# Performance work log

Measured on AMD Instinct MI355X. Metric: run time of the kernel, lower is better.

The kernel has to match this reference:

```python
import jax, jax.numpy as jnp
import numpy as np
from jax import lax

B, T, N, C, AD, HW, KS, KT = 32, 8, 196, 768, 192, 14, 3, 3
EPS = 1e-5

def _groupnorm1(x, gamma, beta, axes):
    # GroupNorm(1, C): normalize over channel+spatial dims per sample
    mu = jnp.mean(x, axis=axes, keepdims=True)
    var = jnp.mean((x - mu) ** 2, axis=axes, keepdims=True)
    xn = (x - mu) * lax.rsqrt(var + EPS)
    shape = [1] * x.ndim
    shape[1] = -1
    return xn * gamma.reshape(shape) + beta.reshape(shape)

def setup_inputs() -> dict:
    key = jax.random.key(0)
    ks = jax.random.split(key, 16)
    s = 0.02
    return {
        'x': jax.random.normal(ks[0], (B, T, N + 1, C), jnp.float32),
        'w_down': jax.random.normal(ks[1], (C, AD), jnp.float32) * s,
        'b_down': jnp.zeros((AD,), jnp.float32),
        'w_sdw': jax.random.normal(ks[2], (AD, 1, KS, KS), jnp.float32) * s,
        'w_spw': jax.random.normal(ks[3], (AD, AD), jnp.float32) * s,  # [out,in]
        'g_snorm': jnp.ones((AD,), jnp.float32),
        'b_snorm': jnp.zeros((AD,), jnp.float32),
        'w_diff': jax.random.normal(ks[4], (AD, AD), jnp.float32) * s,  # [in,out]
        'w_tdw': jax.random.normal(ks[5], (AD, 1, KT), jnp.float32) * s,
        'w_tpw': jax.random.normal(ks[6], (AD, AD), jnp.float32) * s,  # [out,in]
        'g_tnorm': jnp.ones((AD,), jnp.float32),
        'b_tnorm': jnp.zeros((AD,), jnp.float32),
        'w_g1': jax.random.normal(ks[7], (AD, AD), jnp.float32) * s,
        'b_g1': jnp.zeros((AD,), jnp.float32),
        'w_g2': jax.random.normal(ks[8], (AD, AD), jnp.float32) * s,
        'b_g2': jnp.zeros((AD,), jnp.float32),
        'w_up': jax.random.normal(ks[9], (AD, C), jnp.float32) * s,  # torch zero-inits; randomized for nontrivial test
        'b_up': jnp.zeros((C,), jnp.float32),
        'w_cls': jax.random.normal(ks[10], (AD, C), jnp.float32) * s,
        'b_cls': jnp.zeros((C,), jnp.float32),
    }

def reference(x, w_down, b_down, w_sdw, w_spw, g_snorm, b_snorm, w_diff,
              w_tdw, w_tpw, g_tnorm, b_tnorm, w_g1, b_g1, w_g2, b_g2,
              w_up, b_up, w_cls, b_cls):
    gelu = lambda v: jax.nn.gelu(v, approximate=False)  # torch nn.GELU default (erf)
    cls_token = x[:, :, :1, :]
    patch = x[:, :, 1:, :]
    b, t, n, _ = patch.shape
    hw = HW
    ph = patch @ w_down + b_down  # [b,t,n,ad]
    ad = ph.shape[-1]
    # spatial path: (b t) c h w
    sp = ph.reshape(b * t, hw, hw, ad).transpose(0, 3, 1, 2)
    sp = lax.conv_general_dilated(sp, w_sdw, (1, 1), 'SAME',
                                  feature_group_count=ad,
                                  dimension_numbers=('NCHW', 'OIHW', 'NCHW'))
    sp = _groupnorm1(sp, g_snorm, b_snorm, axes=(1, 2, 3))
    sp = gelu(sp)
    sp = jnp.einsum('bchw,oc->bohw', sp, w_spw)
    spatial = sp.transpose(0, 2, 3, 1).reshape(b, t, n, ad)
    # diff gating
    diff = jnp.concatenate([jnp.zeros_like(ph[:, :1]), ph[:, 1:] - ph[:, :-1]], axis=1)
    diff = diff + diff @ w_diff
    # temporal path: (b n) c t
    tp = (ph + diff).transpose(0, 2, 3, 1).reshape(b * n, ad, t)
    tp = lax.conv_general_dilated(tp, w_tdw, (1,), 'SAME',
                                  feature_group_count=ad,
                                  dimension_numbers=('NCH', 'OIH', 'NCH'))
    tp = _groupnorm1(tp, g_tnorm, b_tnorm, axes=(1, 2))
    tp = gelu(tp)
    tp = jnp.einsum('bct,oc->bot', tp, w_tpw)
    temporal = tp.reshape(b, n, ad, t).transpose(0, 3, 1, 2)
    # gate
    gi = jnp.mean(jnp.abs(diff), axis=(1, 2))  # [b, ad]
    gate = jax.nn.sigmoid(gelu(gi @ w_g1 + b_g1) @ w_g2 + b_g2)[:, None, None, :]
    fused = gate * temporal + (1.0 - gate) * spatial
    patch_out = patch + fused @ w_up + b_up
    cls_ctx = jnp.mean(fused, axis=2, keepdims=True)
    cls_out = cls_token + cls_ctx @ w_cls + b_cls
    return jnp.concatenate([cls_out, patch_out], axis=2)
```

## Files before the change

kernel.cpp:

```cpp
#include <hip/hip_runtime.h>
#include <hip/hip_bf16.h>
#include <math.h>

typedef __attribute__((ext_vector_type(8))) short s8v;
typedef __attribute__((ext_vector_type(4))) short s4v;
typedef __attribute__((ext_vector_type(4))) float f4v;

#define GN_EPS 1e-5f

__device__ __forceinline__ float s2f(short s) {
    unsigned int u = ((unsigned int)(unsigned short)s) << 16;
    float f; __builtin_memcpy(&f, &u, 4); return f;
}
__device__ __forceinline__ short f2s(float f) {
    __hip_bfloat16 h = __float2bfloat16(f);
    short s; __builtin_memcpy(&s, &h, 2); return s;
}
__device__ __forceinline__ float gelu_f(float x) {
    return 0.5f * x * (1.0f + erff(x * 0.7071067811865476f));
}
__device__ __forceinline__ s8v lds_load8(const short* p) {
    s8v r;
    *(s4v*)&r       = *(const s4v*)p;
    *((s4v*)&r + 1) = *(const s4v*)(p + 4);
    return r;
}
__device__ __forceinline__ void lds_store8(short* p, s8v v) {
    *(s4v*)p       = *(s4v*)&v;
    *(s4v*)(p + 4) = *((s4v*)&v + 1);
}

__global__ void detect_kernel(const unsigned int* g_snorm_raw, int* flag) {
    if (threadIdx.x == 0) flag[0] = (g_snorm_raw[0] == 0x3F800000u) ? 1 : 0;
}

struct ConvArgs {
    const void* src[19];
    int cum[20];
};
__global__ __launch_bounds__(256)
void convert_kernel(ConvArgs a, short* __restrict__ dst, const int* __restrict__ dflag,
                    int total) {
    const int dt = dflag[0];
    int idx = blockIdx.x * 256 + threadIdx.x;
    const int stride = gridDim.x * 256;
    for (; idx < total; idx += stride) {
        int seg = 0;
        while (idx >= a.cum[seg + 1]) seg++;
        const int off = idx - a.cum[seg];
        const float v = dt ? ((const float*)a.src[seg])[off]
                           : s2f(((const short*)a.src[seg])[off]);
        dst[idx] = f2s(v);
    }
}


#define AMAP_PLAIN 0
#define AMAP_X     1
#define AMAP_DIFF  2
#define EPI_BIASH 0
#define EPI_H     1
#define EPI_DIFF  2
#define EPI_UP    3

template<int K_DIM, int N_DIM, bool B_NK, int AMAP, int EPI>
__global__ __launch_bounds__(256)
void gemm_kernel(const void* __restrict__ Asrc, const short* __restrict__ Bmat,
                 const short* __restrict__ bias, const short* __restrict__ phH,
                 const void* __restrict__ xExt, short* __restrict__ outH,
                 void* __restrict__ outExt, const int* __restrict__ dflag)
{
    const int dt = dflag[0];

    __shared__ short As[64 * 40];
    __shared__ short Bs[64 * 40];

    const int tid  = threadIdx.x;
    const int lane = tid & 63;
    const int wave = tid >> 6;
    const int wr = wave >> 1, wc = wave & 1;
    const int m16 = lane & 15, q = lane >> 4;
    const int rowBase = blockIdx.x * 64;
    const int colBase = blockIdx.y * 64;

    f4v acc[2][2] = {};

    const int ar = tid >> 2;
    const int ak = (tid & 3) * 8;

    for (int k0 = 0; k0 < K_DIM; k0 += 32) {
        {
            s8v av;
            const int grow = rowBase + ar;
            if constexpr (AMAP == AMAP_PLAIN) {
                const short* Ag = (const short*)Asrc;
                av = *(const s8v*)&Ag[(long)grow * K_DIM + k0 + ak];
            } else if constexpr (AMAP == AMAP_X) {
                const int bt = grow / 196;
                const long xi = (long)(grow + bt + 1) * 768 + k0 + ak;
                if (dt) {
                    const float4* q4 = (const float4*)((const float*)Asrc + xi);
                    float4 a = q4[0], b = q4[1];
                    av[0]=f2s(a.x); av[1]=f2s(a.y); av[2]=f2s(a.z); av[3]=f2s(a.w);
                    av[4]=f2s(b.x); av[5]=f2s(b.y); av[6]=f2s(b.z); av[7]=f2s(b.w);
                } else {
                    av = *(const s8v*)((const short*)Asrc + xi);
                }
            } else {
                const short* P = (const short*)Asrc;
                const int bt = grow / 196;
                const int t = bt & 7;
                if (t == 0) {
                    #pragma unroll
                    for (int j = 0; j < 8; j++) av[j] = 0;
                } else {
                    const short* p1 = P + (long)grow * 192 + k0 + ak;
                    const short* p0 = p1 - 196 * 192;
                    #pragma unroll
                    for (int j = 0; j < 8; j++) av[j] = f2s(s2f(p1[j]) - s2f(p0[j]));
                }
            }
            lds_store8(&As[ar * 40 + ak], av);
        }
        if constexpr (B_NK) {
            const int bn = tid >> 2, bk = (tid & 3) * 8;
            s8v bv = *(const s8v*)&Bmat[(long)(colBase + bn) * K_DIM + k0 + bk];
            lds_store8(&Bs[bn * 40 + bk], bv);
        } else {
            const int bk = tid >> 3, bn = (tid & 7) * 8;
            s8v bv = *(const s8v*)&Bmat[(long)(k0 + bk) * N_DIM + colBase + bn];
            #pragma unroll
            for (int j = 0; j < 8; j++) Bs[(bn + j) * 40 + bk] = bv[j];
        }
        __syncthreads();

        s8v afr0 = lds_load8(&As[(wr * 32 + m16) * 40 + q * 8]);
        s8v afr1 = lds_load8(&As[(wr * 32 + 16 + m16) * 40 + q * 8]);
        s8v bfr0 = lds_load8(&Bs[(wc * 32 + m16) * 40 + q * 8]);
        s8v bfr1 = lds_load8(&Bs[(wc * 32 + 16 + m16) * 40 + q * 8]);

        acc[0][0] = __builtin_amdgcn_mfma_f32_16x16x32_bf16(afr0, bfr0, acc[0][0], 0, 0, 0);
        acc[0][1] = __builtin_amdgcn_mfma_f32_16x16x32_bf16(afr0, bfr1, acc[0][1], 0, 0, 0);
        acc[1][0] = __builtin_amdgcn_mfma_f32_16x16x32_bf16(afr1, bfr0, acc[1][0], 0, 0, 0);
        acc[1][1] = __builtin_amdgcn_mfma_f32_16x16x32_bf16(afr1, bfr1, acc[1][1], 0, 0, 0);
        __syncthreads();
    }

    #pragma unroll
    for (int i = 0; i < 2; i++) {
        #pragma unroll
        for (int r = 0; r < 4; r++) {
            const int grow = rowBase + wr * 32 + i * 16 + q * 4 + r;
            #pragma unroll
            for (int j = 0; j < 2; j++) {
                const int gc = colBase + wc * 32 + j * 16 + m16;
                float v = acc[i][j][r];
                if constexpr (EPI == EPI_BIASH) {
                    outH[(long)grow * N_DIM + gc] = f2s(v + s2f(bias[gc]));
                } else if constexpr (EPI == EPI_H) {
                    outH[(long)grow * N_DIM + gc] = f2s(v);
                } else if constexpr (EPI == EPI_DIFF) {
                    const int bt = grow / 196;
                    const int t = bt & 7;
                    const float phv = s2f(phH[(long)grow * 192 + gc]);
                    float d = (t > 0) ? (phv - s2f(phH[(long)(grow - 196) * 192 + gc])) : 0.0f;
                    outH[(long)grow * 192 + gc] = f2s(v + phv + d);
                } else {
                    const int bt = grow / 196;
                    const long oi = (long)(grow + bt + 1) * 768 + gc;
                    const float bv = v + s2f(bias[gc]);
                    if (dt) {
                        ((float*)outExt)[oi] = ((const float*)xExt)[oi] + bv;
                    } else {
                        ((short*)outExt)[oi] = f2s(s2f(((const short*)xExt)[oi]) + bv);
                    }
                }
            }
        }
    }
}

__global__ __launch_bounds__(1024, 4)
void spatial_kernel(const short* __restrict__ ph, const short* __restrict__ w_sdw,
                    const short* __restrict__ g_s, const short* __restrict__ b_s,
                    short* __restrict__ snorm)
{
    __shared__ short tile[196 * 192];
    __shared__ short wkT[9 * 192];
    __shared__ float gsl[192], bsl[192];
    __shared__ float redA[16], redB[16];
    __shared__ float stats[2];

    const int bt = blockIdx.x, tid = threadIdx.x;
    const short* Pg = ph + (long)bt * 37632;

    for (int i = tid; i < 4704; i += 1024)
        *(s8v*)&tile[i * 8] = *(const s8v*)&Pg[i * 8];
    for (int i = tid; i < 1728; i += 1024) {
        const int c = i / 9, tap = i - c * 9;
        wkT[tap * 192 + c] = w_sdw[i];
    }
    if (tid < 192) { gsl[tid] = s2f(g_s[tid]); bsl[tid] = s2f(b_s[tid]); }
    __syncthreads();

    float val[5][8];
    float lsum = 0.f, lsq = 0.f;
    #pragma unroll
    for (int it = 0; it < 5; it++) {
        const int i = tid + it * 1024;
        #pragma unroll
        for (int k = 0; k < 8; k++) val[it][k] = 0.f;
        if (i < 4704) {
            const int n = i / 24, c8 = i - n * 24;
            const int h = n / 14, w = n - (n / 14) * 14;
            float a[8] = {0.f,0.f,0.f,0.f,0.f,0.f,0.f,0.f};
            #pragma unroll
            for (int tap = 0; tap < 9; tap++) {
                const int dh = tap / 3 - 1, dw = tap % 3 - 1;
                const int hh = h + dh, ww = w + dw;
                if (hh >= 0 && hh < 14 && ww >= 0 && ww < 14) {
                    s8v iv = *(const s8v*)&tile[(hh * 14 + ww) * 192 + c8 * 8];
                    s8v wv = *(const s8v*)&wkT[tap * 192 + c8 * 8];
                    #pragma unroll
                    for (int k = 0; k < 8; k++) a[k] += s2f(iv[k]) * s2f(wv[k]);
                }
            }
            #pragma unroll
            for (int k = 0; k < 8; k++) {
                val[it][k] = a[k]; lsum += a[k]; lsq += a[k] * a[k];
            }
        }
    }
    #pragma unroll
    for (int d = 1; d < 64; d <<= 1) {
        lsum += __shfl_xor(lsum, d, 64);
        lsq  += __shfl_xor(lsq,  d, 64);
    }
    if ((tid & 63) == 0) { redA[tid >> 6] = lsum; redB[tid >> 6] = lsq; }
    __syncthreads();
    if (tid < 64) {
        float s = (tid < 16) ? redA[tid] : 0.f;
        float qq = (tid < 16) ? redB[tid] : 0.f;
        #pragma unroll
        for (int d = 1; d < 16; d <<= 1) {
            s  += __shfl_xor(s,  d, 64);
            qq += __shfl_xor(qq, d, 64);
        }
        if (tid == 0) {
            const float inv = 1.0f / 37632.0f;
            const float mean = s * inv;
            const float var  = qq * inv - mean * mean;
            stats[0] = mean; stats[1] = rsqrtf(var + GN_EPS);
        }
    }
    __syncthreads();
    const float mean = stats[0], rstd = stats[1];
    short* Og = snorm + (long)bt * 37632;
    #pragma unroll
    for (int it = 0; it < 5; it++) {
        const int i = tid + it * 1024;
        if (i < 4704) {
            const int c8 = i - (i / 24) * 24;
            s8v o;
            #pragma unroll
            for (int k = 0; k < 8; k++) {
                const int c = c8 * 8 + k;
                const float y = (val[it][k] - mean) * rstd * gsl[c] + bsl[c];
                o[k] = f2s(gelu_f(y));
            }
            *(s8v*)&Og[i * 8] = o;
        }
    }
}

__global__ __launch_bounds__(192)
void gi_kernel(const short* __restrict__ tp, const short* __restrict__ ph,
               float* __restrict__ gi)
{
    const int bt = blockIdx.x;
    const int b = bt >> 3;
    const int tid = threadIdx.x;
    const int c8 = tid >> 3, sub = tid & 7;
    float part[8] = {0.f,0.f,0.f,0.f,0.f,0.f,0.f,0.f};
    for (int n = sub; n < 196; n += 8) {
        const long off = ((long)bt * 196 + n) * 192 + c8 * 8;
        s8v a = *(const s8v*)(tp + off);
        s8v p = *(const s8v*)(ph + off);
        #pragma unroll
        for (int k = 0; k < 8; k++) part[k] += fabsf(s2f(a[k]) - s2f(p[k]));
    }
    #pragma unroll
    for (int d = 1; d < 8; d <<= 1) {
        #pragma unroll
        for (int k = 0; k < 8; k++) part[k] += __shfl_xor(part[k], d, 64);
    }
    if (sub == 0) {
        #pragma unroll
        for (int k = 0; k < 8; k++) atomicAdd(&gi[b * 192 + c8 * 8 + k], part[k]);
    }
}

__global__ __launch_bounds__(192)
void temporal_kernel(const short* __restrict__ tp, const short* __restrict__ w_tdw,
                     const short* __restrict__ g_t, const short* __restrict__ b_t,
                     short* __restrict__ tnorm)
{
    const int bn = blockIdx.x;
    const int c = threadIdx.x;
    const int b = bn / 196, n = bn - (bn / 196) * 196;
    const long base = ((long)b * 8 * 196 + n) * 192 + c;
    const long ts = 196 * 192;
    float v[8], o[8];
    #pragma unroll
    for (int t = 0; t < 8; t++) v[t] = s2f(tp[base + t * ts]);
    const float w0 = s2f(w_tdw[c * 3]), w1 = s2f(w_tdw[c * 3 + 1]), w2 = s2f(w_tdw[c * 3 + 2]);
    #pragma unroll
    for (int t = 0; t < 8; t++) {
        float a = v[t] * w1;
        if (t > 0) a += v[t - 1] * w0;
        if (t < 7) a += v[t + 1] * w2;
        o[t] = a;
    }
    float lsum = 0.f, lsq = 0.f;
    #pragma unroll
    for (int t = 0; t < 8; t++) { lsum += o[t]; lsq += o[t] * o[t]; }
    __shared__ float red1[192], red2[192];
    red1[c] = lsum; red2[c] = lsq;
    __syncthreads();
    for (int s = 96; s > 2; s >>= 1) {
        if (c < s) { red1[c] += red1[c + s]; red2[c] += red2[c + s]; }
        __syncthreads();
    }
    const float mean = (red1[0] + red1[1] + red1[2]) * (1.0f / 1536.0f);
    const float var  = (red2[0] + red2[1] + red2[2]) * (1.0f / 1536.0f) - mean * mean;
    const float rstd = rsqrtf(var + GN_EPS);
    const float gg = s2f(g_t[c]), bb = s2f(b_t[c]);
    #pragma unroll
    for (int t = 0; t < 8; t++) {
        const float y = (o[t] - mean) * rstd * gg + bb;
        tnorm[base + t * ts] = f2s(gelu_f(y));
    }
}

__global__ __launch_bounds__(192)
void gate_kernel(const float* __restrict__ gi, const short* __restrict__ w_g1,
                 const short* __restrict__ b_g1, const short* __restrict__ w_g2,
                 const short* __restrict__ b_g2, float* __restrict__ gate)
{
    const int b = blockIdx.x, o = threadIdx.x;
    __shared__ float s0[192], s1[192];
    s0[o] = gi[b * 192 + o] * (1.0f / 1568.0f);
    __syncthreads();
    float a = s2f(b_g1[o]);
    for (int cc = 0; cc < 192; cc++) a += s0[cc] * s2f(w_g1[cc * 192 + o]);
    s1[o] = gelu_f(a);
    __syncthreads();
    float a2 = s2f(b_g2[o]);
    for (int cc = 0; cc < 192; cc++) a2 += s1[cc] * s2f(w_g2[cc * 192 + o]);
    gate[b * 192 + o] = 1.0f / (1.0f + expf(-a2));
}

__global__ __launch_bounds__(192)
void fuse_kernel(const short* __restrict__ temporal, const short* __restrict__ spatial,
                 const float* __restrict__ gate, short* __restrict__ fused,
                 float* __restrict__ cls_sum)
{
    const int bt = blockIdx.x;
    const int b = bt >> 3;
    const int tid = threadIdx.x;
    const int c8 = tid >> 3, sub = tid & 7;
    float g[8];
    {
        const float4* gp = (const float4*)&gate[b * 192 + c8 * 8];
        float4 ga = gp[0], gb = gp[1];
        g[0]=ga.x; g[1]=ga.y; g[2]=ga.z; g[3]=ga.w;
        g[4]=gb.x; g[5]=gb.y; g[6]=gb.z; g[7]=gb.w;
    }
    float part[8] = {0.f,0.f,0.f,0.f,0.f,0.f,0.f,0.f};
    for (int n = sub; n < 196; n += 8) {
        const long off = ((long)bt * 196 + n) * 192 + c8 * 8;
        s8v tv = *(const s8v*)(temporal + off);
        s8v sv = *(const s8v*)(spatial + off);
        s8v fv;
        #pragma unroll
        for (int k = 0; k < 8; k++) {
            const float f = g[k] * s2f(tv[k]) + (1.0f - g[k]) * s2f(sv[k]);
            fv[k] = f2s(f);
            part[k] += f;
        }
        *(s8v*)(fused + off) = fv;
    }
    #pragma unroll
    for (int d = 1; d < 8; d <<= 1) {
        #pragma unroll
        for (int k = 0; k < 8; k++) part[k] += __shfl_xor(part[k], d, 64);
    }
    if (sub == 0) {
        #pragma unroll
        for (int k = 0; k < 8; k++)
            cls_sum[bt * 192 + c8 * 8 + k] = part[k] * (1.0f / 196.0f);
    }
}

__global__ __launch_bounds__(256)
void cls_kernel(const float* __restrict__ cls_sum, const short* __restrict__ w_cls,
                const short* __restrict__ b_cls, const void* __restrict__ x,
                void* __restrict__ out, const int* __restrict__ dflag)
{
    const int dt = dflag[0];
    const int bt = blockIdx.x, tid = threadIdx.x;
    __shared__ float ctx[192];
    if (tid < 192) ctx[tid] = cls_sum[bt * 192 + tid];
    __syncthreads();
    for (int oc = tid; oc < 768; oc += 256) {
        float a = s2f(b_cls[oc]);
        for (int cc = 0; cc < 192; cc++) a += ctx[cc] * s2f(w_cls[cc * 768 + oc]);
        const long oi = (long)bt * 197 * 768 + oc;
        if (dt) ((float*)out)[oi] = ((const float*)x)[oi] + a;
        else    ((short*)out)[oi] = f2s(s2f(((const short*)x)[oi]) + a);
    }
}

extern "C" void kernel_launch(void* const* d_in, const int* in_sizes, int n_in,
                              void* d_out, int out_size, void* d_ws, size_t ws_size,
                              hipStream_t stream) {
    const void* x = d_in[0];

    const long F = 50176L * 192L;
    short* wsS = (short*)d_ws;
    short* P = wsS;
    short* Q = wsS + F;
    short* R = wsS + 2 * F;
    short* S = wsS + 3 * F;
    short* W = wsS + 4 * F;
    int cum[20]; cum[0] = 0;
    for (int i = 1; i <= 19; i++) cum[i] = cum[i - 1] + in_sizes[i];
    const int totalW = cum[19];
    float* smalls = (float*)(W + ((totalW + 7) & ~7));
    float* gi      = smalls;
    float* gate    = smalls + 6144;
    float* cls_sum = smalls + 12288;
    int*   dflag   = (int*)(smalls + 61440);

    const short* w_down = W + cum[0];
    const short* b_down = W + cum[1];
    const short* w_sdw  = W + cum[2];
    const short* w_spw  = W + cum[3];
    const short* g_sn   = W + cum[4];
    const short* b_sn   = W + cum[5];
    const short* w_diff = W + cum[6];
    const short* w_tdw  = W + cum[7];
    const short* w_tpw  = W + cum[8];
    const short* g_tn   = W + cum[9];
    const short* b_tn   = W + cum[10];
    const short* w_g1   = W + cum[11];
    const short* b_g1   = W + cum[12];
    const short* w_g2   = W + cum[13];
    const short* b_g2   = W + cum[14];
    const short* w_up   = W + cum[15];
    const short* b_up   = W + cum[16];
    const short* w_cls  = W + cum[17];
    const short* b_cls  = W + cum[18];

    hipMemsetAsync(gi, 0, 6144 * sizeof(float), stream);
    detect_kernel<<<1, 64, 0, stream>>>((const unsigned int*)d_in[5], dflag);

    ConvArgs ca;
    for (int i = 0; i < 19; i++) ca.src[i] = d_in[i + 1];
    for (int i = 0; i < 20; i++) ca.cum[i] = cum[i];
    convert_kernel<<<618, 256, 0, stream>>>(ca, W, dflag, totalW);

    dim3 g3(784, 3), g12(784, 12);

    gemm_kernel<768, 192, false, AMAP_X, EPI_BIASH>
        <<<g3, 256, 0, stream>>>(x, w_down, b_down, nullptr, nullptr, P, nullptr, dflag);
    spatial_kernel<<<256, 1024, 0, stream>>>(P, w_sdw, g_sn, b_sn, R);
    gemm_kernel<192, 192, true, AMAP_PLAIN, EPI_H>
        <<<g3, 256, 0, stream>>>(R, w_spw, nullptr, nullptr, nullptr, S, nullptr, dflag);
    gemm_kernel<192, 192, false, AMAP_DIFF, EPI_DIFF>
        <<<g3, 256, 0, stream>>>(P, w_diff, nullptr, P, nullptr, Q, nullptr, dflag);
    gi_kernel<<<256, 192, 0, stream>>>(Q, P, gi);
    temporal_kernel<<<6272, 192, 0, stream>>>(Q, w_tdw, g_tn, b_tn, R);
    gemm_kernel<192, 192, true, AMAP_PLAIN, EPI_H>
        <<<g3, 256, 0, stream>>>(R, w_tpw, nullptr, nullptr, nullptr, Q, nullptr, dflag);
    gate_kernel<<<32, 192, 0, stream>>>(gi, w_g1, b_g1, w_g2, b_g2, gate);
    fuse_kernel<<<256, 192, 0, stream>>>(Q, S, gate, R, cls_sum);
    gemm_kernel<192, 768, false, AMAP_PLAIN, EPI_UP>
        <<<g12, 256, 0, stream>>>(R, w_up, b_up, nullptr, x, nullptr, d_out, dflag);
    cls_kernel<<<256, 256, 0, stream>>>(cls_sum, w_cls, b_cls, x, d_out, dflag);
}
```

Before: 627.8 us.

## Double-buffer GEMM LDS tiles with direct global-to-LDS loads and pre-transposed weights

Rewrites the shared GEMM mainloop to double-buffer the A and B tiles in LDS. The next K-slice is staged with global_load_lds 16-byte transfers while the current slice feeds the MFMAs, and one barrier per iteration replaces two. The padded LDS layout becomes an XOR-swizzled 32-wide layout so fragment reads avoid bank conflicts without padding. Weights that were row-major [K,N] are transposed once per call into [N,K] so every B load is contiguous, which removes the scalar scatter-transpose into LDS. The cost is three extra small transpose launches and more workspace, and mixing direct-to-LDS loads with normal LDS stores relies on correct wave-offset placement.

```diff
diff --git a/kernel.cpp b/kernel.cpp
--- a/kernel.cpp
+++ b/kernel.cpp
@@ -3,7 +3,6 @@
 #include <math.h>
 
 typedef __attribute__((ext_vector_type(8))) short s8v;
-typedef __attribute__((ext_vector_type(4))) short s4v;
 typedef __attribute__((ext_vector_type(4))) float f4v;
 
 #define GN_EPS 1e-5f
@@ -19,15 +18,10 @@
 __device__ __forceinline__ float gelu_f(float x) {
     return 0.5f * x * (1.0f + erff(x * 0.7071067811865476f));
 }
-__device__ __forceinline__ s8v lds_load8(const short* p) {
-    s8v r;
-    *(s4v*)&r       = *(const s4v*)p;
-    *((s4v*)&r + 1) = *(const s4v*)(p + 4);
-    return r;
-}
-__device__ __forceinline__ void lds_store8(short* p, s8v v) {
-    *(s4v*)p       = *(s4v*)&v;
-    *(s4v*)(p + 4) = *((s4v*)&v + 1);
+__device__ __forceinline__ void gload16(const void* g, void* l) {
+    __builtin_amdgcn_global_load_lds((const __attribute__((address_space(1))) void*)g,
+                                     (__attribute__((address_space(3))) void*)l,
+                                     16, 0, 0);
 }
 
 __global__ void detect_kernel(const unsigned int* g_snorm_raw, int* flag) {
@@ -54,6 +48,16 @@
     }
 }
 
+__global__ __launch_bounds__(256)
+void transpose_kernel(const short* __restrict__ src, short* __restrict__ dst,
+                      int R, int C) {
+    const int idx = blockIdx.x * 256 + threadIdx.x;
+    if (idx < R * C) {
+        const int r = idx / C, c = idx - r * C;
+        dst[c * R + r] = src[idx];
+    }
+}
+
 
 #define AMAP_PLAIN 0
 #define AMAP_X     1
@@ -63,7 +67,7 @@
 #define EPI_DIFF  2
 #define EPI_UP    3
 
-template<int K_DIM, int N_DIM, bool B_NK, int AMAP, int EPI>
+template<int K_DIM, int N_DIM, int AMAP, int EPI>
 __global__ __launch_bounds__(256)
 void gemm_kernel(const void* __restrict__ Asrc, const short* __restrict__ Bmat,
                  const short* __restrict__ bias, const short* __restrict__ phH,
@@ -72,8 +76,8 @@
 {
     const int dt = dflag[0];
 
-    __shared__ short As[64 * 40];
-    __shared__ short Bs[64 * 40];
+    __shared__ short As[2][2048];
+    __shared__ short Bs[2][2048];
 
     const int tid  = threadIdx.x;
     const int lane = tid & 63;
@@ -83,67 +87,86 @@
     const int rowBase = blockIdx.x * 64;
     const int colBase = blockIdx.y * 64;
 
+    const int sr = tid >> 2;
+    const int ss = tid & 3;
+    const int sg = ss ^ ((sr >> 1) & 3);
+    const int wOff = wave * 512;
+
+    const int agrow = rowBase + sr;
+    long aBase;
+    int abt7 = 0;
+    if constexpr (AMAP == AMAP_X) {
+        const int bt = agrow / 196;
+        aBase = (long)(agrow + bt + 1) * 768 + sg * 8;
+    } else if constexpr (AMAP == AMAP_DIFF) {
+        aBase = (long)agrow * K_DIM + sg * 8;
+        abt7 = (agrow / 196) & 7;
+    } else {
+        aBase = (long)agrow * K_DIM + sg * 8;
+    }
+    const long bBase = (long)(colBase + sr) * K_DIM + sg * 8;
+
+    const int ra = wr * 32 + m16;
+    const int rb = wc * 32 + m16;
+    const int oA0 = ra * 32 + (q ^ ((ra >> 1) & 3)) * 8;
+    const int oB0 = rb * 32 + (q ^ ((rb >> 1) & 3)) * 8;
+    const int oA1 = oA0 + 512;
+    const int oB1 = oB0 + 512;
+
     f4v acc[2][2] = {};
-
-    const int ar = tid >> 2;
-    const int ak = (tid & 3) * 8;
-
-    for (int k0 = 0; k0 < K_DIM; k0 += 32) {
-        {
+    constexpr int NK = K_DIM / 32;
+
+    auto stage = [&](int kk, int buf) {
+        if constexpr (AMAP == AMAP_PLAIN) {
+            gload16((const short*)Asrc + aBase + kk, (void*)&As[buf][wOff]);
+        } else if constexpr (AMAP == AMAP_X) {
+            if (dt) {
+                const float* xp = (const float*)Asrc + aBase + kk;
+                const float4 f0 = *(const float4*)xp;
+                const float4 f1 = *(const float4*)(xp + 4);
+                s8v av;
+                av[0] = f2s(f0.x); av[1] = f2s(f0.y); av[2] = f2s(f0.z); av[3] = f2s(f0.w);
+                av[4] = f2s(f1.x); av[5] = f2s(f1.y); av[6] = f2s(f1.z); av[7] = f2s(f1.w);
+                *(s8v*)&As[buf][sr * 32 + ss * 8] = av;
+            } else {
+                gload16((const short*)Asrc + aBase + kk, (void*)&As[buf][wOff]);
+            }
+        } else {
             s8v av;
-            const int grow = rowBase + ar;
-            if constexpr (AMAP == AMAP_PLAIN) {
-                const short* Ag = (const short*)Asrc;
-                av = *(const s8v*)&Ag[(long)grow * K_DIM + k0 + ak];
-            } else if constexpr (AMAP == AMAP_X) {
-                const int bt = grow / 196;
-                const long xi = (long)(grow + bt + 1) * 768 + k0 + ak;
-                if (dt) {
-                    const float4* q4 = (const float4*)((const float*)Asrc + xi);
-                    float4 a = q4[0], b = q4[1];
-                    av[0]=f2s(a.x); av[1]=f2s(a.y); av[2]=f2s(a.z); av[3]=f2s(a.w);
-                    av[4]=f2s(b.x); av[5]=f2s(b.y); av[6]=f2s(b.z); av[7]=f2s(b.w);
-                } else {
-                    av = *(const s8v*)((const short*)Asrc + xi);
-                }
+            if (abt7) {
+                const short* p1 = (const short*)Asrc + aBase + kk;
+                const s8v v1 = *(const s8v*)p1;
+                const s8v v0 = *(const s8v*)(p1 - 37632);
+                #pragma unroll
+                for (int j = 0; j < 8; j++) av[j] = f2s(s2f(v1[j]) - s2f(v0[j]));
             } else {
-                const short* P = (const short*)Asrc;
-                const int bt = grow / 196;
-                const int t = bt & 7;
-                if (t == 0) {
-                    #pragma unroll
-                    for (int j = 0; j < 8; j++) av[j] = 0;
-                } else {
-                    const short* p1 = P + (long)grow * 192 + k0 + ak;
-                    const short* p0 = p1 - 196 * 192;
-                    #pragma unroll
-                    for (int j = 0; j < 8; j++) av[j] = f2s(s2f(p1[j]) - s2f(p0[j]));
-                }
+                #pragma unroll
+                for (int j = 0; j < 8; j++) av[j] = 0;
             }
-            lds_store8(&As[ar * 40 + ak], av);
-        }
-        if constexpr (B_NK) {
-            const int bn = tid >> 2, bk = (tid & 3) * 8;
-            s8v bv = *(const s8v*)&Bmat[(long)(colBase + bn) * K_DIM + k0 + bk];
-            lds_store8(&Bs[bn * 40 + bk], bv);
-        } else {
-            const int bk = tid >> 3, bn = (tid & 7) * 8;
-            s8v bv = *(const s8v*)&Bmat[(long)(k0 + bk) * N_DIM + colBase + bn];
-            #pragma unroll
-            for (int j = 0; j < 8; j++) Bs[(bn + j) * 40 + bk] = bv[j];
-        }
-        __syncthreads();
-
-        s8v afr0 = lds_load8(&As[(wr * 32 + m16) * 40 + q * 8]);
-        s8v afr1 = lds_load8(&As[(wr * 32 + 16 + m16) * 40 + q * 8]);
-        s8v bfr0 = lds_load8(&Bs[(wc * 32 + m16) * 40 + q * 8]);
-        s8v bfr1 = lds_load8(&Bs[(wc * 32 + 16 + m16) * 40 + q * 8]);
+            *(s8v*)&As[buf][sr * 32 + ss * 8] = av;
+        }
+        gload16(Bmat + bBase + kk, (void*)&Bs[buf][wOff]);
+    };
+
+    stage(0, 0);
+    __syncthreads();
+
+    int cur = 0;
+    for (int t = 0; t < NK; ++t) {
+        if (t + 1 < NK) stage((t + 1) * 32, cur ^ 1);
+
+        const s8v afr0 = *(const s8v*)&As[cur][oA0];
+        const s8v afr1 = *(const s8v*)&As[cur][oA1];
+        const s8v bfr0 = *(const s8v*)&Bs[cur][oB0];
+        const s8v bfr1 = *(const s8v*)&Bs[cur][oB1];
 
         acc[0][0] = __builtin_amdgcn_mfma_f32_16x16x32_bf16(afr0, bfr0, acc[0][0], 0, 0, 0);
         acc[0][1] = __builtin_amdgcn_mfma_f32_16x16x32_bf16(afr0, bfr1, acc[0][1], 0, 0, 0);
         acc[1][0] = __builtin_amdgcn_mfma_f32_16x16x32_bf16(afr1, bfr0, acc[1][0], 0, 0, 0);
         acc[1][1] = __builtin_amdgcn_mfma_f32_16x16x32_bf16(afr1, bfr1, acc[1][1], 0, 0, 0);
+
         __syncthreads();
+        cur ^= 1;
     }
 
     #pragma unroll
@@ -436,19 +459,23 @@
     int cum[20]; cum[0] = 0;
     for (int i = 1; i <= 19; i++) cum[i] = cum[i - 1] + in_sizes[i];
     const int totalW = cum[19];
-    float* smalls = (float*)(W + ((totalW + 7) & ~7));
+
+    short* WT   = W + ((totalW + 7) & ~7);
+    short* wdT  = WT;
+    short* wdfT = WT + 147456;
+    short* wupT = WT + 147456 + 36864;
+
+    float* smalls = (float*)(WT + 331776);
     float* gi      = smalls;
     float* gate    = smalls + 6144;
     float* cls_sum = smalls + 12288;
     int*   dflag   = (int*)(smalls + 61440);
 
-    const short* w_down = W + cum[0];
     const short* b_down = W + cum[1];
     const short* w_sdw  = W + cum[2];
     const short* w_spw  = W + cum[3];
     const short* g_sn   = W + cum[4];
     const short* b_sn   = W + cum[5];
-    const short* w_diff = W + cum[6];
     const short* w_tdw  = W + cum[7];
     const short* w_tpw  = W + cum[8];
     const short* g_tn   = W + cum[9];
@@ -457,7 +484,6 @@
     const short* b_g1   = W + cum[12];
     const short* w_g2   = W + cum[13];
     const short* b_g2   = W + cum[14];
-    const short* w_up   = W + cum[15];
     const short* b_up   = W + cum[16];
     const short* w_cls  = W + cum[17];
     const short* b_cls  = W + cum[18];
@@ -470,22 +496,26 @@
     for (int i = 0; i < 20; i++) ca.cum[i] = cum[i];
     convert_kernel<<<618, 256, 0, stream>>>(ca, W, dflag, totalW);
 
+    transpose_kernel<<<576, 256, 0, stream>>>(W + cum[0],  wdT,  768, 192);
+    transpose_kernel<<<144, 256, 0, stream>>>(W + cum[6],  wdfT, 192, 192);
+    transpose_kernel<<<576, 256, 0, stream>>>(W + cum[15], wupT, 192, 768);
+
     dim3 g3(784, 3), g12(784, 12);
 
-    gemm_kernel<768, 192, false, AMAP_X, EPI_BIASH>
-        <<<g3, 256, 0, stream>>>(x, w_down, b_down, nullptr, nullptr, P, nullptr, dflag);
+    gemm_kernel<768, 192, AMAP_X, EPI_BIASH>
+        <<<g3, 256, 0, stream>>>(x, wdT, b_down, nullptr, nullptr, P, nullptr, dflag);
     spatial_kernel<<<256, 1024, 0, stream>>>(P, w_sdw, g_sn, b_sn, R);
-    gemm_kernel<192, 192, true, AMAP_PLAIN, EPI_H>
+    gemm_kernel<192, 192, AMAP_PLAIN, EPI_H>
         <<<g3, 256, 0, stream>>>(R, w_spw, nullptr, nullptr, nullptr, S, nullptr, dflag);
-    gemm_kernel<192, 192, false, AMAP_DIFF, EPI_DIFF>
-        <<<g3, 256, 0, stream>>>(P, w_diff, nullptr, P, nullptr, Q, nullptr, dflag);
+    gemm_kernel<192, 192, AMAP_DIFF, EPI_DIFF>
+        <<<g3, 256, 0, stream>>>(P, wdfT, nullptr, P, nullptr, Q, nullptr, dflag);
     gi_kernel<<<256, 192, 0, stream>>>(Q, P, gi);
     temporal_kernel<<<6272, 192, 0, stream>>>(Q, w_tdw, g_tn, b_tn, R);
-    gemm_kernel<192, 192, true, AMAP_PLAIN, EPI_H>
+    gemm_kernel<192, 192, AMAP_PLAIN, EPI_H>
         <<<g3, 256, 0, stream>>>(R, w_tpw, nullptr, nullptr, nullptr, Q, nullptr, dflag);
     gate_kernel<<<32, 192, 0, stream>>>(gi, w_g1, b_g1, w_g2, b_g2, gate);
     fuse_kernel<<<256, 192, 0, stream>>>(Q, S, gate, R, cls_sum);
-    gemm_kernel<192, 768, false, AMAP_PLAIN, EPI_UP>
-        <<<g12, 256, 0, stream>>>(R, w_up, b_up, nullptr, x, nullptr, d_out, dflag);
+    gemm_kernel<192, 768, AMAP_PLAIN, EPI_UP>
+        <<<g12, 256, 0, stream>>>(R, wupT, b_up, nullptr, x, nullptr, d_out, dflag);
     cls_kernel<<<256, 256, 0, stream>>>(cls_sum, w_cls, b_cls, x, d_out, dflag);
 }
```

Measured after the change: 607.4 us. 1.03x faster.
